# Optimization experiments

Hardware: AMD Instinct MI355X
Metric: run time of the kernel (lower is better)

## Reference

```python
import jax, jax.numpy as jnp
import numpy as np

B, S, E, H = 2, 2048, 1024, 16
D = E // H  # head_dim = 64


def setup_inputs() -> dict:
    key = jax.random.key(0)
    ks = jax.random.split(key, 6)
    sc = 0.02
    return {
        "hidden_states": jax.random.normal(ks[0], (B, S, E), dtype=jnp.float32),
        "attn_bias": jax.random.normal(ks[1], (S, S), dtype=jnp.float32) * sc,
        "Wqkv": jax.random.normal(ks[2], (E, 3 * E), dtype=jnp.float32) * sc,
        "bqkv": jax.random.normal(ks[3], (3 * E,), dtype=jnp.float32) * sc,
        "Wproj": jax.random.normal(ks[4], (E, E), dtype=jnp.float32) * sc,
        "bproj": jax.random.normal(ks[5], (E,), dtype=jnp.float32) * sc,
    }


def reference(hidden_states, attn_bias, Wqkv, bqkv, Wproj, bproj):
    b, s, e = hidden_states.shape
    qkv = hidden_states @ Wqkv + bqkv                      # [b,s,3e]
    q, k, v = jnp.split(qkv, 3, axis=-1)                   # each [b,s,e]
    cache_key, cache_value = k, v                          # kvCache
    # [b,h,s,d]
    qh = q.reshape(b, s, H, D).transpose(0, 2, 1, 3)
    kh = k.reshape(b, s, H, D).transpose(0, 2, 1, 3)
    vh = v.reshape(b, s, H, D).transpose(0, 2, 1, 3)
    scores = jnp.einsum("bhqd,bhkd->bhqk", qh, kh) / jnp.sqrt(jnp.float32(D))
    scores = scores + attn_bias[:s, :s][None, None]        # learned additive bias
    causal = jnp.tril(jnp.ones((s, s), dtype=bool))
    scores = jnp.where(causal[None, None], scores, jnp.float32(-1e9))
    attn = jax.nn.softmax(scores, axis=-1)
    ctx = jnp.einsum("bhqk,bhkd->bhqd", attn, vh)
    ctx = ctx.transpose(0, 2, 1, 3).reshape(b, s, e)
    out = ctx @ Wproj + bproj                              # resid dropout p=0 -> identity
    return (out, cache_key, cache_value)
```

## Files before the change

### kernel.cpp

```cpp
#include <hip/hip_runtime.h>

#define B_ 2
#define S_ 2048
#define E_ 1024
#define H_ 16
#define D_ 64

typedef short  s16x8 __attribute__((ext_vector_type(8)));
typedef float  f32x4 __attribute__((ext_vector_type(4)));
typedef unsigned short u16x4 __attribute__((ext_vector_type(4)));

__device__ __forceinline__ ushort f2bf(float f) {
    union { float f; unsigned u; } x; x.f = f;
    unsigned u = x.u + 0x7fffu + ((x.u >> 16) & 1u);
    return (ushort)(u >> 16);
}

__global__ __launch_bounds__(256) void cvtx_kernel(
    const float* __restrict__ X, ushort* __restrict__ Xbf)
{
    int i = (blockIdx.x * 256 + threadIdx.x) * 4;
    float4 v = *(const float4*)&X[i];
    u16x4 o;
    o.x = f2bf(v.x); o.y = f2bf(v.y); o.z = f2bf(v.z); o.w = f2bf(v.w);
    *(u16x4*)&Xbf[i] = o;
}

__global__ __launch_bounds__(256) void wtrans_kernel(
    const float* __restrict__ W, ushort* __restrict__ Wt, int Kdim, int Ndim)
{
    __shared__ float tile[64][65];
    int n0 = blockIdx.x * 64, k0 = blockIdx.y * 64;
    int tid = threadIdx.x;
    int c = tid & 63;
#pragma unroll
    for (int r = tid >> 6; r < 64; r += 4)
        tile[r][c] = W[(size_t)(k0 + r) * Ndim + n0 + c];
    __syncthreads();
#pragma unroll
    for (int r = tid >> 6; r < 64; r += 4)
        Wt[(size_t)(n0 + r) * Kdim + k0 + c] = f2bf(tile[c][r]);
}

__global__ __launch_bounds__(256) void gemm_mfma_bt(
    const ushort* __restrict__ A,
    const ushort* __restrict__ Bt,
    const float* __restrict__ bias,
    int M, int N, int K,
    float* __restrict__ C0,
    ushort* __restrict__ Qbf, float* __restrict__ Kf32, ushort* __restrict__ Kbf,
    float* __restrict__ Vf32, int mode)
{
    __shared__ ushort As[128 * 32];
    __shared__ ushort Bs[128 * 32];
    int tid = threadIdx.x;
    int wid = tid >> 6, lane = tid & 63;
    int l15 = lane & 15, quad = lane >> 4;
    int wm = wid >> 1, wn = wid & 1;
    int row0 = blockIdx.y * 128, col0 = blockIdx.x * 128;

    int sr = wid * 16 + (lane >> 2);
    int sk = (lane & 3) * 8;

    f32x4 acc[4][4];
#pragma unroll
    for (int mt = 0; mt < 4; mt++)
#pragma unroll
        for (int nt = 0; nt < 4; nt++) acc[mt][nt] = (f32x4){0.f, 0.f, 0.f, 0.f};

    for (int k0 = 0; k0 < K; k0 += 32) {
        __syncthreads();
#pragma unroll
        for (int c = 0; c < 2; c++) {
            int r = c * 64 + sr;
            __builtin_amdgcn_global_load_lds(
                (const __attribute__((address_space(1))) unsigned int*)
                    &A[(size_t)(row0 + r) * K + k0 + sk],
                (__attribute__((address_space(3))) unsigned int*)&As[r * 32 + sk],
                16, 0, 0);
            __builtin_amdgcn_global_load_lds(
                (const __attribute__((address_space(1))) unsigned int*)
                    &Bt[(size_t)(col0 + r) * K + k0 + sk],
                (__attribute__((address_space(3))) unsigned int*)&Bs[r * 32 + sk],
                16, 0, 0);
        }
        __syncthreads();

        s16x8 af[4], bf[4];
#pragma unroll
        for (int mt = 0; mt < 4; mt++)
            af[mt] = *(const s16x8*)&As[(wm * 64 + mt * 16 + l15) * 32 + quad * 8];
#pragma unroll
        for (int nt = 0; nt < 4; nt++)
            bf[nt] = *(const s16x8*)&Bs[(wn * 64 + nt * 16 + l15) * 32 + quad * 8];
#pragma unroll
        for (int mt = 0; mt < 4; mt++)
#pragma unroll
            for (int nt = 0; nt < 4; nt++)
                acc[mt][nt] = __builtin_amdgcn_mfma_f32_16x16x32_bf16(
                    af[mt], bf[nt], acc[mt][nt], 0, 0, 0);
    }

#pragma unroll
    for (int nt = 0; nt < 4; nt++) {
        int n = col0 + wn * 64 + nt * 16 + l15;
        float bv = bias[n];
        if (mode == 1) {
            int seg = n >> 10;
            int nn = n & (E_ - 1);
#pragma unroll
            for (int mt = 0; mt < 4; mt++)
#pragma unroll
                for (int r = 0; r < 4; r++) {
                    int row = row0 + wm * 64 + mt * 16 + quad * 4 + r;
                    float v = acc[mt][nt][r] + bv;
                    size_t idx = (size_t)row * E_ + nn;
                    if (seg == 0)      Qbf[idx] = f2bf(v);
                    else if (seg == 1) { Kf32[idx] = v; Kbf[idx] = f2bf(v); }
                    else               Vf32[idx] = v;
                }
        } else {
#pragma unroll
            for (int mt = 0; mt < 4; mt++)
#pragma unroll
                for (int r = 0; r < 4; r++) {
                    int row = row0 + wm * 64 + mt * 16 + quad * 4 + r;
                    C0[(size_t)row * N + n] = acc[mt][nt][r] + bv;
                }
        }
    }
}

__global__ __launch_bounds__(256) void vtrans_kernel(
    const float* __restrict__ V, ushort* __restrict__ Vt)
{
    __shared__ float tile[64][65];
    int blk = blockIdx.x;
    int s0 = (blk & 31) * 64;
    int bh = blk >> 5;
    int b = bh >> 4, h = bh & 15;
    int tid = threadIdx.x;
    int d = tid & 63;
#pragma unroll
    for (int i = tid >> 6; i < 64; i += 4)
        tile[i][d] = V[((size_t)(b * S_ + s0 + i)) * E_ + h * 64 + d];
    __syncthreads();
    int lane = tid & 63, w = tid >> 6;
#pragma unroll
    for (int dd = w; dd < 64; dd += 4)
        Vt[((size_t)(bh * 64 + dd)) * S_ + s0 + lane] = f2bf(tile[lane][dd]);
}

__global__ __launch_bounds__(256) void attn_mfma_kernel(
    const ushort* __restrict__ Qbf,
    const ushort* __restrict__ Kbf,
    const ushort* __restrict__ Vt,
    const float* __restrict__ bias,
    ushort* __restrict__ Ctx)
{
    __shared__ ushort Ks[64][72];
    __shared__ ushort Vs[64][72];
    __shared__ ushort Ps[4][16][72];

    int blk = blockIdx.x;
    int bh = blk & 31;
    int pr = blk >> 5;
    int b = bh >> 4, h = bh & 15;
    int tid = threadIdx.x;
    int wid = tid >> 6, lane = tid & 63;
    int l15 = lane & 15, quad = lane >> 4;

    int skey = tid >> 2;
    int scol = (tid & 3) * 16;
    const float scale = 0.125f;

    const size_t krow = (size_t)(b * S_ + skey) * E_ + h * 64 + scol;
    const size_t vrow = (size_t)(bh * 64 + skey) * S_ + scol;

    for (int half = 0; half < 2; half++) {
        int qt = half ? pr : (31 - pr);
        int q0w = qt * 64 + wid * 16;

        const size_t qbase = ((size_t)(b * S_ + q0w + l15)) * E_ + h * 64 + quad * 8;
        s16x8 qa0 = *(const s16x8*)&Qbf[qbase];
        s16x8 qa1 = *(const s16x8*)&Qbf[qbase + 32];

        f32x4 o[4];
#pragma unroll
        for (int dt = 0; dt < 4; dt++) o[dt] = (f32x4){0.f, 0.f, 0.f, 0.f};
        float lsum[4];
#pragma unroll
        for (int r = 0; r < 4; r++) lsum[r] = 0.f;

        float4 kr0 = ((const float4*)&Kbf[krow])[0];
        float4 kr1 = ((const float4*)&Kbf[krow])[1];
        float4 vr0 = ((const float4*)&Vt[vrow])[0];
        float4 vr1 = ((const float4*)&Vt[vrow])[1];
        float bvn[4][4];
#pragma unroll
        for (int r = 0; r < 4; r++)
#pragma unroll
            for (int kt = 0; kt < 4; kt++)
                bvn[r][kt] = bias[(size_t)(q0w + quad * 4 + r) * S_ + kt * 16 + l15];

        for (int t = 0; t <= qt; t++) {
            int j0 = t * 64;
            __syncthreads();
            *(float4*)&Ks[skey][scol]     = kr0;
            *(float4*)&Ks[skey][scol + 8] = kr1;
            *(float4*)&Vs[skey][scol]     = vr0;
            *(float4*)&Vs[skey][scol + 8] = vr1;
            float bv[4][4];
#pragma unroll
            for (int r = 0; r < 4; r++)
#pragma unroll
                for (int kt = 0; kt < 4; kt++) bv[r][kt] = bvn[r][kt];
            __syncthreads();

            if (t < qt) {
                int j1 = j0 + 64;
                kr0 = ((const float4*)&Kbf[krow + (size_t)j1 * E_])[0];
                kr1 = ((const float4*)&Kbf[krow + (size_t)j1 * E_])[1];
                vr0 = ((const float4*)&Vt[vrow + j1])[0];
                vr1 = ((const float4*)&Vt[vrow + j1])[1];
#pragma unroll
                for (int r = 0; r < 4; r++)
#pragma unroll
                    for (int kt = 0; kt < 4; kt++)
                        bvn[r][kt] = bias[(size_t)(q0w + quad * 4 + r) * S_ + j1 + kt * 16 + l15];
            }

            f32x4 s[4];
#pragma unroll
            for (int kt = 0; kt < 4; kt++) {
                s16x8 kb0 = *(const s16x8*)&Ks[kt * 16 + l15][quad * 8];
                s16x8 kb1 = *(const s16x8*)&Ks[kt * 16 + l15][quad * 8 + 32];
                f32x4 acc = (f32x4){0.f, 0.f, 0.f, 0.f};
                acc = __builtin_amdgcn_mfma_f32_16x16x32_bf16(qa0, kb0, acc, 0, 0, 0);
                acc = __builtin_amdgcn_mfma_f32_16x16x32_bf16(qa1, kb1, acc, 0, 0, 0);
                s[kt] = acc;
            }

            bool diag = (t == qt);
#pragma unroll
            for (int r = 0; r < 4; r++) {
                int row = q0w + quad * 4 + r;
#pragma unroll
                for (int kt = 0; kt < 4; kt++) {
                    int j = j0 + kt * 16 + l15;
                    float v = s[kt][r] * scale + bv[r][kt];
                    float p = (diag && j > row) ? 0.f : __expf(v);
                    lsum[r] += p;
                    int chunk = (kt * 2 + (l15 >> 3)) ^ quad;
                    Ps[wid][quad * 4 + r][chunk * 8 + (l15 & 7)] = f2bf(p);
                }
            }

            int cb = (quad ^ (l15 >> 2)) * 8;
            s16x8 pa0 = *(const s16x8*)&Ps[wid][l15][cb];
            s16x8 pa1 = *(const s16x8*)&Ps[wid][l15][cb + 32];
#pragma unroll
            for (int dt = 0; dt < 4; dt++) {
                s16x8 vb0 = *(const s16x8*)&Vs[dt * 16 + l15][quad * 8];
                s16x8 vb1 = *(const s16x8*)&Vs[dt * 16 + l15][quad * 8 + 32];
                o[dt] = __builtin_amdgcn_mfma_f32_16x16x32_bf16(pa0, vb0, o[dt], 0, 0, 0);
                o[dt] = __builtin_amdgcn_mfma_f32_16x16x32_bf16(pa1, vb1, o[dt], 0, 0, 0);
            }
        }

        float inv_l[4];
#pragma unroll
        for (int r = 0; r < 4; r++) {
            float l = lsum[r];
            l += __shfl_xor(l, 1);
            l += __shfl_xor(l, 2);
            l += __shfl_xor(l, 4);
            l += __shfl_xor(l, 8);
            inv_l[r] = 1.f / l;
        }

#pragma unroll
        for (int dt = 0; dt < 4; dt++) {
#pragma unroll
            for (int r = 0; r < 4; r++) {
                int row = q0w + quad * 4 + r;
                Ctx[((size_t)(b * S_ + row)) * E_ + h * 64 + dt * 16 + l15] =
                    f2bf(o[dt][r] * inv_l[r]);
            }
        }
    }
}

extern "C" void kernel_launch(void* const* d_in, const int* in_sizes, int n_in,
                              void* d_out, int out_size, void* d_ws, size_t ws_size,
                              hipStream_t stream) {
    const float* X     = (const float*)d_in[0];
    const float* abias = (const float*)d_in[1];
    const float* Wqkv  = (const float*)d_in[2];
    const float* bqkv  = (const float*)d_in[3];
    const float* Wproj = (const float*)d_in[4];
    const float* bproj = (const float*)d_in[5];

    const size_t plane = (size_t)B_ * S_ * E_;
    float* out  = (float*)d_out;
    float* kout = out + plane;
    float* vout = kout + plane;

    ushort* xbf    = (ushort*)d_ws;
    ushort* qbf    = xbf + plane;
    ushort* kbf    = qbf + plane;
    ushort* vt     = kbf + plane;
    ushort* ctxbf  = xbf;
    ushort* wqkvt  = vt + plane;
    ushort* wprojt = wqkvt + (size_t)3 * E_ * E_;

    const int M = B_ * S_;

    cvtx_kernel<<<dim3(plane / 1024), 256, 0, stream>>>(X, xbf);
    wtrans_kernel<<<dim3(3 * E_ / 64, E_ / 64), 256, 0, stream>>>(Wqkv, wqkvt, E_, 3 * E_);
    wtrans_kernel<<<dim3(E_ / 64, E_ / 64), 256, 0, stream>>>(Wproj, wprojt, E_, E_);

    gemm_mfma_bt<<<dim3(3 * E_ / 128, M / 128), 256, 0, stream>>>(
        xbf, wqkvt, bqkv, M, 3 * E_, E_,
        nullptr, qbf, kout, kbf, vout, 1);

    vtrans_kernel<<<dim3(B_ * H_ * (S_ / 64)), 256, 0, stream>>>(vout, vt);

    attn_mfma_kernel<<<dim3(B_ * H_ * 16), 256, 0, stream>>>(
        qbf, kbf, vt, abias, ctxbf);

    gemm_mfma_bt<<<dim3(E_ / 128, M / 128), 256, 0, stream>>>(
        ctxbf, wprojt, bproj, M, E_, E_,
        out, nullptr, nullptr, nullptr, nullptr, 0);
}
```

Before: 238.2 us.

## Enlarge attention query tile to 128 rows and fuse prep kernels

The attention kernel now gives each block 128 query rows instead of 64, with each wave computing two 16-row MFMA tiles. This reuses every K/V tile staged in shared memory across twice as many queries. It also computes scores transposed (K as the A operand) so the bias can be read as float4 vectors and P written to LDS as packed u16x4. The three preprocessing kernels are merged into one launch to cut launch overhead. The cost is that the grid halves to 256 blocks, which lowers parallelism and may leave compute units idle, and register pressure per wave rises.

After: 262.2 us. 10.0% more time.

```diff
diff --git a/kernel.cpp b/kernel.cpp
--- a/kernel.cpp
+++ b/kernel.cpp
@@ -16,22 +16,32 @@
     return (ushort)(u >> 16);
 }
 
-__global__ __launch_bounds__(256) void cvtx_kernel(
-    const float* __restrict__ X, ushort* __restrict__ Xbf)
-{
-    int i = (blockIdx.x * 256 + threadIdx.x) * 4;
-    float4 v = *(const float4*)&X[i];
-    u16x4 o;
-    o.x = f2bf(v.x); o.y = f2bf(v.y); o.z = f2bf(v.z); o.w = f2bf(v.w);
-    *(u16x4*)&Xbf[i] = o;
-}
-
-__global__ __launch_bounds__(256) void wtrans_kernel(
-    const float* __restrict__ W, ushort* __restrict__ Wt, int Kdim, int Ndim)
+__global__ __launch_bounds__(256) void prep_kernel(
+    const float* __restrict__ X, ushort* __restrict__ Xbf,
+    const float* __restrict__ Wqkv, ushort* __restrict__ Wqkvt,
+    const float* __restrict__ Wproj, ushort* __restrict__ Wprojt)
 {
     __shared__ float tile[64][65];
-    int n0 = blockIdx.x * 64, k0 = blockIdx.y * 64;
+    int blk = blockIdx.x;
     int tid = threadIdx.x;
+    if (blk < 4096) {
+        int i = blk * 1024 + tid * 4;
+        float4 v = *(const float4*)&X[i];
+        u16x4 o;
+        o.x = f2bf(v.x); o.y = f2bf(v.y); o.z = f2bf(v.z); o.w = f2bf(v.w);
+        *(u16x4*)&Xbf[i] = o;
+        return;
+    }
+    const float* W; ushort* Wt; int Kdim, Ndim, n0, k0;
+    if (blk < 4096 + 768) {
+        int bb = blk - 4096;
+        W = Wqkv; Wt = Wqkvt; Kdim = E_; Ndim = 3 * E_;
+        n0 = (bb % 48) * 64; k0 = (bb / 48) * 64;
+    } else {
+        int bb = blk - 4864;
+        W = Wproj; Wt = Wprojt; Kdim = E_; Ndim = E_;
+        n0 = (bb % 16) * 64; k0 = (bb / 16) * 64;
+    }
     int c = tid & 63;
 #pragma unroll
     for (int r = tid >> 6; r < 64; r += 4)
@@ -160,7 +170,7 @@
 {
     __shared__ ushort Ks[64][72];
     __shared__ ushort Vs[64][72];
-    __shared__ ushort Ps[4][16][72];
+    __shared__ ushort Ps[4][32][72];
 
     int blk = blockIdx.x;
     int bh = blk & 31;
@@ -178,114 +188,127 @@
     const size_t vrow = (size_t)(bh * 64 + skey) * S_ + scol;
 
     for (int half = 0; half < 2; half++) {
-        int qt = half ? pr : (31 - pr);
-        int q0w = qt * 64 + wid * 16;
-
-        const size_t qbase = ((size_t)(b * S_ + q0w + l15)) * E_ + h * 64 + quad * 8;
-        s16x8 qa0 = *(const s16x8*)&Qbf[qbase];
-        s16x8 qa1 = *(const s16x8*)&Qbf[qbase + 32];
-
-        f32x4 o[4];
-#pragma unroll
-        for (int dt = 0; dt < 4; dt++) o[dt] = (f32x4){0.f, 0.f, 0.f, 0.f};
-        float lsum[4];
-#pragma unroll
-        for (int r = 0; r < 4; r++) lsum[r] = 0.f;
+        int qt = half ? pr : (15 - pr);
+        int q0w = qt * 128 + wid * 32;
+        int ntiles = 2 * qt + 2;
+
+        s16x8 qa0[2], qa1[2];
+#pragma unroll
+        for (int m = 0; m < 2; m++) {
+            size_t qb = (size_t)(b * S_ + q0w + m * 16 + l15) * E_ + h * 64 + quad * 8;
+            qa0[m] = *(const s16x8*)&Qbf[qb];
+            qa1[m] = *(const s16x8*)&Qbf[qb + 32];
+        }
+
+        f32x4 o[2][4];
+#pragma unroll
+        for (int m = 0; m < 2; m++)
+#pragma unroll
+            for (int dt = 0; dt < 4; dt++) o[m][dt] = (f32x4){0.f, 0.f, 0.f, 0.f};
+        float lsum[2] = {0.f, 0.f};
 
         float4 kr0 = ((const float4*)&Kbf[krow])[0];
         float4 kr1 = ((const float4*)&Kbf[krow])[1];
         float4 vr0 = ((const float4*)&Vt[vrow])[0];
         float4 vr1 = ((const float4*)&Vt[vrow])[1];
-        float bvn[4][4];
-#pragma unroll
-        for (int r = 0; r < 4; r++)
+        f32x4 bvn[2][4];
+#pragma unroll
+        for (int m = 0; m < 2; m++)
 #pragma unroll
             for (int kt = 0; kt < 4; kt++)
-                bvn[r][kt] = bias[(size_t)(q0w + quad * 4 + r) * S_ + kt * 16 + l15];
-
-        for (int t = 0; t <= qt; t++) {
+                bvn[m][kt] = *(const f32x4*)&bias[(size_t)(q0w + m * 16 + l15) * S_ + kt * 16 + quad * 4];
+
+        for (int t = 0; t < ntiles; t++) {
             int j0 = t * 64;
             __syncthreads();
             *(float4*)&Ks[skey][scol]     = kr0;
             *(float4*)&Ks[skey][scol + 8] = kr1;
             *(float4*)&Vs[skey][scol]     = vr0;
             *(float4*)&Vs[skey][scol + 8] = vr1;
-            float bv[4][4];
-#pragma unroll
-            for (int r = 0; r < 4; r++)
-#pragma unroll
-                for (int kt = 0; kt < 4; kt++) bv[r][kt] = bvn[r][kt];
             __syncthreads();
 
-            if (t < qt) {
+            if (t + 1 < ntiles) {
                 int j1 = j0 + 64;
                 kr0 = ((const float4*)&Kbf[krow + (size_t)j1 * E_])[0];
                 kr1 = ((const float4*)&Kbf[krow + (size_t)j1 * E_])[1];
                 vr0 = ((const float4*)&Vt[vrow + j1])[0];
                 vr1 = ((const float4*)&Vt[vrow + j1])[1];
-#pragma unroll
-                for (int r = 0; r < 4; r++)
-#pragma unroll
-                    for (int kt = 0; kt < 4; kt++)
-                        bvn[r][kt] = bias[(size_t)(q0w + quad * 4 + r) * S_ + j1 + kt * 16 + l15];
-            }
-
-            f32x4 s[4];
+            }
+
+            f32x4 s[2][4];
 #pragma unroll
             for (int kt = 0; kt < 4; kt++) {
                 s16x8 kb0 = *(const s16x8*)&Ks[kt * 16 + l15][quad * 8];
                 s16x8 kb1 = *(const s16x8*)&Ks[kt * 16 + l15][quad * 8 + 32];
-                f32x4 acc = (f32x4){0.f, 0.f, 0.f, 0.f};
-                acc = __builtin_amdgcn_mfma_f32_16x16x32_bf16(qa0, kb0, acc, 0, 0, 0);
-                acc = __builtin_amdgcn_mfma_f32_16x16x32_bf16(qa1, kb1, acc, 0, 0, 0);
-                s[kt] = acc;
-            }
-
-            bool diag = (t == qt);
-#pragma unroll
-            for (int r = 0; r < 4; r++) {
-                int row = q0w + quad * 4 + r;
+#pragma unroll
+                for (int m = 0; m < 2; m++) {
+                    f32x4 a = (f32x4){0.f, 0.f, 0.f, 0.f};
+                    a = __builtin_amdgcn_mfma_f32_16x16x32_bf16(kb0, qa0[m], a, 0, 0, 0);
+                    s[m][kt] = __builtin_amdgcn_mfma_f32_16x16x32_bf16(kb1, qa1[m], a, 0, 0, 0);
+                }
+            }
+
+            bool diag = (t >= 2 * qt);
+#pragma unroll
+            for (int m = 0; m < 2; m++) {
+                int row = q0w + m * 16 + l15;
 #pragma unroll
                 for (int kt = 0; kt < 4; kt++) {
-                    int j = j0 + kt * 16 + l15;
-                    float v = s[kt][r] * scale + bv[r][kt];
-                    float p = (diag && j > row) ? 0.f : __expf(v);
-                    lsum[r] += p;
-                    int chunk = (kt * 2 + (l15 >> 3)) ^ quad;
-                    Ps[wid][quad * 4 + r][chunk * 8 + (l15 & 7)] = f2bf(p);
-                }
-            }
-
-            int cb = (quad ^ (l15 >> 2)) * 8;
-            s16x8 pa0 = *(const s16x8*)&Ps[wid][l15][cb];
-            s16x8 pa1 = *(const s16x8*)&Ps[wid][l15][cb + 32];
+                    f32x4 bb = bvn[m][kt];
+                    u16x4 pk;
+#pragma unroll
+                    for (int r = 0; r < 4; r++) {
+                        int j = j0 + kt * 16 + quad * 4 + r;
+                        float v = s[m][kt][r] * scale + bb[r];
+                        float p = (diag && j > row) ? 0.f : __expf(v);
+                        lsum[m] += p;
+                        pk[r] = f2bf(p);
+                    }
+                    *(u16x4*)&Ps[wid][m * 16 + l15][kt * 16 + quad * 4] = pk;
+                }
+            }
+
+            if (t + 1 < ntiles) {
+                int j1 = j0 + 64;
+#pragma unroll
+                for (int m = 0; m < 2; m++)
+#pragma unroll
+                    for (int kt = 0; kt < 4; kt++)
+                        bvn[m][kt] = *(const f32x4*)&bias[(size_t)(q0w + m * 16 + l15) * S_ + j1 + kt * 16 + quad * 4];
+            }
+
+            s16x8 pa0[2], pa1[2];
+#pragma unroll
+            for (int m = 0; m < 2; m++) {
+                pa0[m] = *(const s16x8*)&Ps[wid][m * 16 + l15][quad * 8];
+                pa1[m] = *(const s16x8*)&Ps[wid][m * 16 + l15][quad * 8 + 32];
+            }
 #pragma unroll
             for (int dt = 0; dt < 4; dt++) {
                 s16x8 vb0 = *(const s16x8*)&Vs[dt * 16 + l15][quad * 8];
                 s16x8 vb1 = *(const s16x8*)&Vs[dt * 16 + l15][quad * 8 + 32];
-                o[dt] = __builtin_amdgcn_mfma_f32_16x16x32_bf16(pa0, vb0, o[dt], 0, 0, 0);
-                o[dt] = __builtin_amdgcn_mfma_f32_16x16x32_bf16(pa1, vb1, o[dt], 0, 0, 0);
-            }
-        }
-
-        float inv_l[4];
-#pragma unroll
-        for (int r = 0; r < 4; r++) {
-            float l = lsum[r];
-            l += __shfl_xor(l, 1);
-            l += __shfl_xor(l, 2);
-            l += __shfl_xor(l, 4);
-            l += __shfl_xor(l, 8);
-            inv_l[r] = 1.f / l;
-        }
-
-#pragma unroll
-        for (int dt = 0; dt < 4; dt++) {
+#pragma unroll
+                for (int m = 0; m < 2; m++) {
+                    o[m][dt] = __builtin_amdgcn_mfma_f32_16x16x32_bf16(pa0[m], vb0, o[m][dt], 0, 0, 0);
+                    o[m][dt] = __builtin_amdgcn_mfma_f32_16x16x32_bf16(pa1[m], vb1, o[m][dt], 0, 0, 0);
+                }
+            }
+        }
+
+#pragma unroll
+        for (int m = 0; m < 2; m++) {
+            float l = lsum[m];
+            l += __shfl_xor(l, 16);
+            l += __shfl_xor(l, 32);
+            float inv = 1.f / l;
 #pragma unroll
             for (int r = 0; r < 4; r++) {
-                int row = q0w + quad * 4 + r;
-                Ctx[((size_t)(b * S_ + row)) * E_ + h * 64 + dt * 16 + l15] =
-                    f2bf(o[dt][r] * inv_l[r]);
+                float invr = __shfl(inv, quad * 4 + r);
+                int row = q0w + m * 16 + quad * 4 + r;
+#pragma unroll
+                for (int dt = 0; dt < 4; dt++)
+                    Ctx[((size_t)(b * S_ + row)) * E_ + h * 64 + dt * 16 + l15] =
+                        f2bf(o[m][dt][r] * invr);
             }
         }
     }
@@ -316,9 +339,8 @@
 
     const int M = B_ * S_;
 
-    cvtx_kernel<<<dim3(plane / 1024), 256, 0, stream>>>(X, xbf);
-    wtrans_kernel<<<dim3(3 * E_ / 64, E_ / 64), 256, 0, stream>>>(Wqkv, wqkvt, E_, 3 * E_);
-    wtrans_kernel<<<dim3(E_ / 64, E_ / 64), 256, 0, stream>>>(Wproj, wprojt, E_, E_);
+    prep_kernel<<<dim3(4096 + 768 + 256), 256, 0, stream>>>(
+        X, xbf, Wqkv, wqkvt, Wproj, wprojt);
 
     gemm_mfma_bt<<<dim3(3 * E_ / 128, M / 128), 256, 0, stream>>>(
         xbf, wqkvt, bqkv, M, 3 * E_, E_,
@@ -326,7 +348,7 @@
 
     vtrans_kernel<<<dim3(B_ * H_ * (S_ / 64)), 256, 0, stream>>>(vout, vt);
 
-    attn_mfma_kernel<<<dim3(B_ * H_ * 16), 256, 0, stream>>>(
+    attn_mfma_kernel<<<dim3(B_ * H_ * 8), 256, 0, stream>>>(
         qbf, kbf, vt, abias, ctxbf);
 
     gemm_mfma_bt<<<dim3(E_ / 128, M / 128), 256, 0, stream>>>(
```
